# Performance work log

Measured on AMD Instinct MI355X. Metric: run time of the kernel, lower is better.

Reference implementation:

```python
import jax, jax.numpy as jnp
import numpy as np

N_NODES = 100000
N_EDGES = 600000
FEAT = 128
N_RELS = 8


def setup_inputs() -> dict:
    key = jax.random.key(0)
    k1, k2, k3, k4, k5, k6, k7 = jax.random.split(key, 7)
    return {
        "h": jax.random.normal(k1, (N_NODES, FEAT), dtype=jnp.float32),
        "weight": jax.random.normal(k2, (N_RELS, FEAT, FEAT), dtype=jnp.float32) * (1.0 / np.sqrt(FEAT)),
        "gate_weight": jax.random.normal(k3, (N_RELS, FEAT, 1), dtype=jnp.float32) * (1.0 / np.sqrt(FEAT)),
        "norm": jax.random.uniform(k4, (N_EDGES, 1), dtype=jnp.float32),
        "src": jax.random.randint(k5, (N_EDGES,), 0, N_NODES, dtype=jnp.int32),
        "dst": jax.random.randint(k6, (N_EDGES,), 0, N_NODES, dtype=jnp.int32),
        "rel_type": jax.random.randint(k7, (N_EDGES,), 0, N_RELS, dtype=jnp.int32),
    }


def reference(h, weight, gate_weight, norm, src, dst, rel_type):
    # Transform every node by every relation once: [N, R, F].
    # Mathematically identical to per-edge bmm h_src @ W[rel], but avoids
    # materializing an [E, F, F] gathered weight tensor.
    h_all = jnp.einsum('nd,rdf->nrf', h, weight)            # [N, R, F]
    gate_all = jnp.einsum('nd,rdo->nro', h, gate_weight)[..., 0]  # [N, R]

    msg = h_all[src, rel_type] * norm                        # [E, F]
    gate = jax.nn.sigmoid(gate_all[src, rel_type])[:, None]  # [E, 1]
    msg = msg * gate

    out = jax.ops.segment_sum(msg, dst, num_segments=h.shape[0])  # scatter-sum to dst nodes
    return jax.nn.relu(out)
```

## Files before the change

### kernel.cpp

```cpp
#include <hip/hip_runtime.h>
#include <hip/hip_bf16.h>

#define FEAT 128
#define NRELS 8
#define KTOT 1024
#define BN 32
#define ECAP 256
#define CPAD 16

typedef __bf16 bf16_t;
typedef __bf16 bf16x2_t __attribute__((ext_vector_type(2)));
typedef __bf16 bf16x8_t __attribute__((ext_vector_type(8)));
typedef float f32x4 __attribute__((ext_vector_type(4)));

struct __align__(8) PackedEdge { int row; float scale; };

static inline size_t align256(size_t x) { return (x + 255) & ~(size_t)255; }

__global__ __launch_bounds__(256) void k_prep(
    const float* __restrict__ h, const float* __restrict__ gwt,
    const float* __restrict__ w, float* __restrict__ sg,
    bf16_t* __restrict__ hb, bf16_t* __restrict__ wt2,
    int* __restrict__ cur, int N, int nbk) {
    const int t = threadIdx.x;
    const int gid = blockIdx.x * 256 + t;
    const int nthreads = gridDim.x * 256;
    for (int i = gid; i < NRELS * FEAT * FEAT; i += nthreads) {
        int r = i >> 14;
        int rem = i & 16383;
        int d = rem >> 7;
        int f = rem & 127;
        wt2[(size_t)f * KTOT + r * FEAT + d] = (bf16_t)w[i];
    }
    for (int i = gid; i < nbk * CPAD + 1; i += nthreads) cur[i] = 0;

    const int gw_id = gid >> 6;
    const int nwaves = nthreads >> 6;
    const int lane = t & 63;
    for (int node = gw_id; node < N; node += nwaves) {
        float2 hv2 = *reinterpret_cast<const float2*>(h + (size_t)node * FEAT + lane * 2);
        bf16x2_t hc;
        hc.x = (bf16_t)hv2.x;
        hc.y = (bf16_t)hv2.y;
        *reinterpret_cast<bf16x2_t*>(hb + (size_t)node * FEAT + lane * 2) = hc;

        int r = lane >> 3;
        int g = lane & 7;
        const float4* hp = reinterpret_cast<const float4*>(h + (size_t)node * FEAT + g * 16);
        const float4* wp = reinterpret_cast<const float4*>(gwt + r * FEAT + g * 16);
        float s = 0.f;
#pragma unroll
        for (int i = 0; i < 4; ++i) {
            float4 a = hp[i];
            float4 b = wp[i];
            s += a.x * b.x + a.y * b.y + a.z * b.z + a.w * b.w;
        }
        s += __shfl_xor(s, 1, 64);
        s += __shfl_xor(s, 2, 64);
        s += __shfl_xor(s, 4, 64);
        if (g == 0) sg[(size_t)node * NRELS + r] = 1.0f / (1.0f + __expf(-s));
    }
}

__global__ void k_fills(const int* __restrict__ src, const int* __restrict__ dstv,
                        const int* __restrict__ rel, const float* __restrict__ nrm,
                        const float* __restrict__ sg, int* __restrict__ cur,
                        PackedEdge* __restrict__ slab, PackedEdge* __restrict__ ovfrec,
                        int* __restrict__ ovfbk, int* __restrict__ ovfcnt, int nedges) {
    int e = blockIdx.x * blockDim.x + threadIdx.x;
    if (e >= nedges) return;
    int d = dstv[e];
    int s = src[e];
    int r = rel[e];
    int bk = d >> 5;
    PackedEdge p;
    p.row = (s << 8) | ((d & 31) << 3) | r;
    p.scale = nrm[e] * sg[(size_t)s * NRELS + r];
    int pos = atomicAdd(&cur[bk * CPAD], 1);
    if (pos < ECAP) {
        slab[(size_t)bk * ECAP + pos] = p;
    } else {
        int op = atomicAdd(ovfcnt, 1);
        ovfrec[op] = p;
        ovfbk[op] = bk;
    }
}

__global__ __launch_bounds__(512, 4) void k_aggemm(const bf16_t* __restrict__ hb,
                                                   const bf16_t* __restrict__ wt2,
                                                   const PackedEdge* __restrict__ slab,
                                                   const int* __restrict__ cur,
                                                   const PackedEdge* __restrict__ ovfrec,
                                                   const int* __restrict__ ovfbk,
                                                   const int* __restrict__ ovfcnt,
                                                   float* __restrict__ out, int nnodes) {
    __shared__ __align__(16) char lds_raw[BN * KTOT * sizeof(bf16_t)];
    __shared__ __align__(8) PackedEdge elist[ECAP];
    __shared__ int kcnt[256];
    __shared__ int kbase[257];
    __shared__ int kwork[256];
    float* cst = (float*)lds_raw;
    const int t = threadIdx.x;
    const int nb0 = blockIdx.x * BN;
    const int lane = t & 63;
    const int wv = t >> 6;
    const int l15 = lane & 15;
    const int lhi = lane >> 4;

    const bf16_t* bp = wt2 + (size_t)(wv * 16 + l15) * KTOT + lhi * 8;
    bf16x8_t bv0 = *reinterpret_cast<const bf16x8_t*>(bp);
    bf16x8_t bv1 = *reinterpret_cast<const bf16x8_t*>(bp + 32);
    bf16x8_t bv2 = *reinterpret_cast<const bf16x8_t*>(bp + 64);
    bf16x8_t bv3 = *reinterpret_cast<const bf16x8_t*>(bp + 96);

    {
        f32x4 z = {0.f, 0.f, 0.f, 0.f};
#pragma unroll
        for (int i = 0; i < 8; ++i)
            reinterpret_cast<f32x4*>(lds_raw)[t + i * 512] = z;
    }

    const int cnt = cur[blockIdx.x * CPAD];
    const int nE = cnt < ECAP ? cnt : ECAP;
    if (t < 256) kcnt[t] = 0;
    __syncthreads();

    PackedEdge myrec = {0, 0.f};
    if (t < nE) {
        myrec = slab[(size_t)blockIdx.x * ECAP + t];
        atomicAdd(&kcnt[myrec.row & 255], 1);
    }
    __syncthreads();

    if (t < 64) {
        int c0 = kcnt[t * 4], c1 = kcnt[t * 4 + 1];
        int c2 = kcnt[t * 4 + 2], c3 = kcnt[t * 4 + 3];
        int tot = c0 + c1 + c2 + c3;
        int incl = tot;
#pragma unroll
        for (int off = 1; off < 64; off <<= 1) {
            int y = __shfl_up(incl, off, 64);
            if (t >= off) incl += y;
        }
        int excl = incl - tot;
        kbase[t * 4] = excl;               kwork[t * 4] = excl;
        kbase[t * 4 + 1] = excl + c0;      kwork[t * 4 + 1] = excl + c0;
        kbase[t * 4 + 2] = excl + c0 + c1; kwork[t * 4 + 2] = excl + c0 + c1;
        kbase[t * 4 + 3] = excl + c0 + c1 + c2;
        kwork[t * 4 + 3] = excl + c0 + c1 + c2;
        if (t == 63) kbase[256] = excl + tot;
    }
    __syncthreads();

    if (t < nE) elist[atomicAdd(&kwork[myrec.row & 255], 1)] = myrec;
    __syncthreads();

    {
        const int g2 = t >> 3;
        const int node = g2 >> 1;
        const int cidx = ((g2 & 1) << 3) | (t & 7);
        const int sw = node & 15;
        const int jbeg = kbase[node * 8];
        const int jend = kbase[node * 8 + 8];
        if (jbeg < jend) {
            float a[8];
#pragma unroll
            for (int i = 0; i < 8; ++i) a[i] = 0.f;
            int cur_r;

            auto ldrec = [&](int idx) {
                return elist[idx < jend ? idx : jend - 1];
            };
            auto ldrow = [&](const PackedEdge& p) {
                return *reinterpret_cast<const bf16x8_t*>(
                    hb + ((size_t)(p.row >> 8) << 7) + cidx * 8);
            };
            auto flush = [&](int rr) {
                int chunk = (rr * 16 + cidx) ^ sw;
                bf16_t* dp = reinterpret_cast<bf16_t*>(
                    lds_raw + (size_t)node * 2048 + chunk * 16);
                bf16x8_t old = *reinterpret_cast<const bf16x8_t*>(dp);
                bf16x8_t o;
#pragma unroll
                for (int i = 0; i < 8; ++i) o[i] = (bf16_t)((float)old[i] + a[i]);
                *reinterpret_cast<bf16x8_t*>(dp) = o;
            };
            auto consume = [&](const PackedEdge& p, const bf16x8_t& v, int idx) {
                if (idx < jend) {
                    int r = p.row & 7;
                    if (r != cur_r) {
                        flush(cur_r);
#pragma unroll
                        for (int i = 0; i < 8; ++i) a[i] = 0.f;
                        cur_r = r;
                    }
                    float s = p.scale;
#pragma unroll
                    for (int i = 0; i < 8; ++i) a[i] += (float)v[i] * s;
                }
            };

            PackedEdge p0 = ldrec(jbeg), p1 = ldrec(jbeg + 1);
            PackedEdge p2 = ldrec(jbeg + 2), p3 = ldrec(jbeg + 3);
            PackedEdge q0 = ldrec(jbeg + 4), q1 = ldrec(jbeg + 5);
            PackedEdge q2 = ldrec(jbeg + 6), q3 = ldrec(jbeg + 7);
            bf16x8_t v0 = ldrow(p0);
            bf16x8_t v1 = ldrow(p1);
            bf16x8_t v2 = ldrow(p2);
            bf16x8_t v3 = ldrow(p3);
            cur_r = p0.row & 7;

#pragma unroll 1
            for (int j = jbeg; j < jend; j += 4) {
                PackedEdge r0 = ldrec(j + 8), r1 = ldrec(j + 9);
                PackedEdge r2 = ldrec(j + 10), r3 = ldrec(j + 11);
                consume(p0, v0, j);
                consume(p1, v1, j + 1);
                consume(p2, v2, j + 2);
                consume(p3, v3, j + 3);
                v0 = ldrow(q0); v1 = ldrow(q1); v2 = ldrow(q2); v3 = ldrow(q3);
                p0 = q0; p1 = q1; p2 = q2; p3 = q3;
                q0 = r0; q1 = r1; q2 = r2; q3 = r3;
            }
            flush(cur_r);
        }

        int novf = *ovfcnt;
        if (novf > 0) {
#pragma unroll 1
            for (int i = 0; i < novf; ++i) {
                if (ovfbk[i] != blockIdx.x) continue;
                PackedEdge p = ovfrec[i];
                if (((p.row >> 3) & 31) != node) continue;
                bf16x8_t v = *reinterpret_cast<const bf16x8_t*>(
                    hb + ((size_t)(p.row >> 8) << 7) + cidx * 8);
                int chunk = ((p.row & 7) * 16 + cidx) ^ sw;
                bf16_t* dp = reinterpret_cast<bf16_t*>(
                    lds_raw + (size_t)node * 2048 + chunk * 16);
                bf16x8_t old = *reinterpret_cast<const bf16x8_t*>(dp);
                bf16x8_t o;
#pragma unroll
                for (int k = 0; k < 8; ++k)
                    o[k] = (bf16_t)((float)old[k] + (float)v[k] * p.scale);
                *reinterpret_cast<bf16x8_t*>(dp) = o;
            }
        }
    }
    __syncthreads();

    f32x4 acc0 = {0.f, 0.f, 0.f, 0.f};
    f32x4 acc1 = {0.f, 0.f, 0.f, 0.f};
    const char* a0p = lds_raw + (size_t)l15 * 2048;
    const char* a1p = a0p + 16 * 2048;
    const int swb = l15;

#define PB_STEP(I, BV)                                                         \
    {                                                                          \
        int ks = ks0 + (I);                                                    \
        int coff = ((ks * 4 + lhi) ^ swb) << 4;                                \
        bf16x8_t av0 = *reinterpret_cast<const bf16x8_t*>(a0p + coff);         \
        bf16x8_t av1 = *reinterpret_cast<const bf16x8_t*>(a1p + coff);         \
        bf16x8_t nxt = *reinterpret_cast<const bf16x8_t*>(                     \
            bp + (((ks + 4) & 31) * 32));                                      \
        acc0 = __builtin_amdgcn_mfma_f32_16x16x32_bf16(av0, BV, acc0, 0, 0, 0);\
        acc1 = __builtin_amdgcn_mfma_f32_16x16x32_bf16(av1, BV, acc1, 0, 0, 0);\
        BV = nxt;                                                              \
    }

#pragma unroll 1
    for (int ks0 = 0; ks0 < 32; ks0 += 4) {
        PB_STEP(0, bv0)
        PB_STEP(1, bv1)
        PB_STEP(2, bv2)
        PB_STEP(3, bv3)
    }
#undef PB_STEP
    __syncthreads();

    {
        int f = wv * 16 + l15;
#pragma unroll
        for (int i = 0; i < 4; ++i) {
            int n0 = lhi * 4 + i;
            cst[n0 * 132 + f] = acc0[i];
            cst[(n0 + 16) * 132 + f] = acc1[i];
        }
    }
    __syncthreads();

    {
        int node = t >> 4;
        int f0 = (t & 15) * 8;
        int gnode = nb0 + node;
        if (gnode < nnodes) {
            const float* cr = cst + node * 132 + f0;
            float4 o0, o1;
            o0.x = fmaxf(cr[0], 0.f); o0.y = fmaxf(cr[1], 0.f);
            o0.z = fmaxf(cr[2], 0.f); o0.w = fmaxf(cr[3], 0.f);
            o1.x = fmaxf(cr[4], 0.f); o1.y = fmaxf(cr[5], 0.f);
            o1.z = fmaxf(cr[6], 0.f); o1.w = fmaxf(cr[7], 0.f);
            float4* op = reinterpret_cast<float4*>(out + (size_t)gnode * FEAT + f0);
            op[0] = o0;
            op[1] = o1;
        }
    }
}

extern "C" void kernel_launch(void* const* d_in, const int* in_sizes, int n_in,
                              void* d_out, int out_size, void* d_ws, size_t ws_size,
                              hipStream_t stream) {
    const float* h = (const float*)d_in[0];
    const float* w = (const float*)d_in[1];
    const float* gwt = (const float*)d_in[2];
    const float* nrm = (const float*)d_in[3];
    const int* src = (const int*)d_in[4];
    const int* dst = (const int*)d_in[5];
    const int* rel = (const int*)d_in[6];
    float* out = (float*)d_out;

    const int N = in_sizes[0] / FEAT;
    const int E = in_sizes[4];
    const int nbk = (N + BN - 1) / BN;

    char* ws = (char*)d_ws;
    const size_t wt2B = align256((size_t)FEAT * KTOT * sizeof(bf16_t));
    const size_t hbB  = align256((size_t)N * FEAT * sizeof(bf16_t));
    const size_t sgB  = align256((size_t)N * NRELS * sizeof(float));
    const size_t cuB  = align256(((size_t)nbk * CPAD + 1) * sizeof(int));
    const size_t slB  = align256((size_t)nbk * ECAP * sizeof(PackedEdge));
    const size_t ovB  = align256((size_t)E * sizeof(PackedEdge));

    bf16_t* wt2 = (bf16_t*)ws;
    bf16_t* hb = (bf16_t*)(ws + wt2B);
    float* sg = (float*)(ws + wt2B + hbB);
    int* cur = (int*)(ws + wt2B + hbB + sgB);
    int* ovfcnt = cur + (size_t)nbk * CPAD;
    PackedEdge* slab = (PackedEdge*)(ws + wt2B + hbB + sgB + cuB);
    PackedEdge* ovfrec = (PackedEdge*)(ws + wt2B + hbB + sgB + cuB + slB);
    int* ovfbk = (int*)(ws + wt2B + hbB + sgB + cuB + slB + ovB);

    k_prep<<<4096, 256, 0, stream>>>(h, gwt, w, sg, hb, wt2, cur, N, nbk);
    k_fills<<<(E + 255) / 256, 256, 0, stream>>>(src, dst, rel, nrm, sg, cur, slab,
                                                 ovfrec, ovfbk, ovfcnt, E);
    k_aggemm<<<nbk, 512, 0, stream>>>(hb, wt2, slab, cur, ovfrec, ovfbk, ovfcnt,
                                      out, N);
}
```

Baseline: 294.0 us.

## Halve destination-node tile to 16 and rework gather lanes and weight transpose

Shrinks the per-block destination tile from 32 to 16 nodes, with a smaller edge capacity and a 7-bit row packing. Each wave now does one MFMA accumulator instead of two, and the gather gives each node 32 lanes that each load 4 bf16 values. This halves LDS per block so more blocks fit per CU and the grid grows, at the cost of reloading the 1024x128 weight fragments for twice as many blocks. The weight-transpose prep loop now writes contiguously and reads strided.

```diff
diff --git a/kernel.cpp b/kernel.cpp
--- a/kernel.cpp
+++ b/kernel.cpp
@@ -4,12 +4,13 @@
 #define FEAT 128
 #define NRELS 8
 #define KTOT 1024
-#define BN 32
-#define ECAP 256
+#define BN 16
+#define ECAP 192
 #define CPAD 16
 
 typedef __bf16 bf16_t;
 typedef __bf16 bf16x2_t __attribute__((ext_vector_type(2)));
+typedef __bf16 bf16x4_t __attribute__((ext_vector_type(4)));
 typedef __bf16 bf16x8_t __attribute__((ext_vector_type(8)));
 typedef float f32x4 __attribute__((ext_vector_type(4)));
 
@@ -26,11 +27,11 @@
     const int gid = blockIdx.x * 256 + t;
     const int nthreads = gridDim.x * 256;
     for (int i = gid; i < NRELS * FEAT * FEAT; i += nthreads) {
-        int r = i >> 14;
-        int rem = i & 16383;
-        int d = rem >> 7;
-        int f = rem & 127;
-        wt2[(size_t)f * KTOT + r * FEAT + d] = (bf16_t)w[i];
+        int f = i >> 10;
+        int k = i & 1023;
+        int r = k >> 7;
+        int d = k & 127;
+        wt2[i] = (bf16_t)w[(r << 14) + (d << 7) + f];
     }
     for (int i = gid; i < nbk * CPAD + 1; i += nthreads) cur[i] = 0;
 
@@ -72,9 +73,9 @@
     int d = dstv[e];
     int s = src[e];
     int r = rel[e];
-    int bk = d >> 5;
+    int bk = d >> 4;
     PackedEdge p;
-    p.row = (s << 8) | ((d & 31) << 3) | r;
+    p.row = (s << 7) | ((d & 15) << 3) | r;
     p.scale = nrm[e] * sg[(size_t)s * NRELS + r];
     int pos = atomicAdd(&cur[bk * CPAD], 1);
     if (pos < ECAP) {
@@ -96,9 +97,9 @@
                                                    float* __restrict__ out, int nnodes) {
     __shared__ __align__(16) char lds_raw[BN * KTOT * sizeof(bf16_t)];
     __shared__ __align__(8) PackedEdge elist[ECAP];
-    __shared__ int kcnt[256];
-    __shared__ int kbase[257];
-    __shared__ int kwork[256];
+    __shared__ int kcnt[128];
+    __shared__ int kbase[129];
+    __shared__ int kwork[128];
     float* cst = (float*)lds_raw;
     const int t = threadIdx.x;
     const int nb0 = blockIdx.x * BN;
@@ -116,26 +117,25 @@
     {
         f32x4 z = {0.f, 0.f, 0.f, 0.f};
 #pragma unroll
-        for (int i = 0; i < 8; ++i)
+        for (int i = 0; i < 4; ++i)
             reinterpret_cast<f32x4*>(lds_raw)[t + i * 512] = z;
     }
 
     const int cnt = cur[blockIdx.x * CPAD];
     const int nE = cnt < ECAP ? cnt : ECAP;
-    if (t < 256) kcnt[t] = 0;
+    if (t < 128) kcnt[t] = 0;
     __syncthreads();
 
     PackedEdge myrec = {0, 0.f};
     if (t < nE) {
         myrec = slab[(size_t)blockIdx.x * ECAP + t];
-        atomicAdd(&kcnt[myrec.row & 255], 1);
+        atomicAdd(&kcnt[myrec.row & 127], 1);
     }
     __syncthreads();
 
     if (t < 64) {
-        int c0 = kcnt[t * 4], c1 = kcnt[t * 4 + 1];
-        int c2 = kcnt[t * 4 + 2], c3 = kcnt[t * 4 + 3];
-        int tot = c0 + c1 + c2 + c3;
+        int c0 = kcnt[t * 2], c1 = kcnt[t * 2 + 1];
+        int tot = c0 + c1;
         int incl = tot;
 #pragma unroll
         for (int off = 1; off < 64; off <<= 1) {
@@ -143,60 +143,56 @@
             if (t >= off) incl += y;
         }
         int excl = incl - tot;
-        kbase[t * 4] = excl;               kwork[t * 4] = excl;
-        kbase[t * 4 + 1] = excl + c0;      kwork[t * 4 + 1] = excl + c0;
-        kbase[t * 4 + 2] = excl + c0 + c1; kwork[t * 4 + 2] = excl + c0 + c1;
-        kbase[t * 4 + 3] = excl + c0 + c1 + c2;
-        kwork[t * 4 + 3] = excl + c0 + c1 + c2;
-        if (t == 63) kbase[256] = excl + tot;
-    }
-    __syncthreads();
-
-    if (t < nE) elist[atomicAdd(&kwork[myrec.row & 255], 1)] = myrec;
+        kbase[t * 2] = excl;          kwork[t * 2] = excl;
+        kbase[t * 2 + 1] = excl + c0; kwork[t * 2 + 1] = excl + c0;
+        if (t == 63) kbase[128] = excl + tot;
+    }
+    __syncthreads();
+
+    if (t < nE) elist[atomicAdd(&kwork[myrec.row & 127], 1)] = myrec;
     __syncthreads();
 
     {
-        const int g2 = t >> 3;
-        const int node = g2 >> 1;
-        const int cidx = ((g2 & 1) << 3) | (t & 7);
-        const int sw = node & 15;
+        const int node = t >> 5;
+        const int c8 = t & 31;
+        const int sw = node;
         const int jbeg = kbase[node * 8];
         const int jend = kbase[node * 8 + 8];
         if (jbeg < jend) {
-            float a[8];
-#pragma unroll
-            for (int i = 0; i < 8; ++i) a[i] = 0.f;
+            float a[4];
+#pragma unroll
+            for (int i = 0; i < 4; ++i) a[i] = 0.f;
             int cur_r;
 
             auto ldrec = [&](int idx) {
                 return elist[idx < jend ? idx : jend - 1];
             };
             auto ldrow = [&](const PackedEdge& p) {
-                return *reinterpret_cast<const bf16x8_t*>(
-                    hb + ((size_t)(p.row >> 8) << 7) + cidx * 8);
+                return *reinterpret_cast<const bf16x4_t*>(
+                    hb + ((size_t)(p.row >> 7) << 7) + c8 * 4);
             };
             auto flush = [&](int rr) {
-                int chunk = (rr * 16 + cidx) ^ sw;
+                int chunk = (rr * 16 + (c8 >> 1)) ^ sw;
                 bf16_t* dp = reinterpret_cast<bf16_t*>(
-                    lds_raw + (size_t)node * 2048 + chunk * 16);
-                bf16x8_t old = *reinterpret_cast<const bf16x8_t*>(dp);
-                bf16x8_t o;
-#pragma unroll
-                for (int i = 0; i < 8; ++i) o[i] = (bf16_t)((float)old[i] + a[i]);
-                *reinterpret_cast<bf16x8_t*>(dp) = o;
+                    lds_raw + (size_t)node * 2048 + chunk * 16 + (c8 & 1) * 8);
+                bf16x4_t old = *reinterpret_cast<const bf16x4_t*>(dp);
+                bf16x4_t o;
+#pragma unroll
+                for (int i = 0; i < 4; ++i) o[i] = (bf16_t)((float)old[i] + a[i]);
+                *reinterpret_cast<bf16x4_t*>(dp) = o;
             };
-            auto consume = [&](const PackedEdge& p, const bf16x8_t& v, int idx) {
+            auto consume = [&](const PackedEdge& p, const bf16x4_t& v, int idx) {
                 if (idx < jend) {
                     int r = p.row & 7;
                     if (r != cur_r) {
                         flush(cur_r);
 #pragma unroll
-                        for (int i = 0; i < 8; ++i) a[i] = 0.f;
+                        for (int i = 0; i < 4; ++i) a[i] = 0.f;
                         cur_r = r;
                     }
                     float s = p.scale;
 #pragma unroll
-                    for (int i = 0; i < 8; ++i) a[i] += (float)v[i] * s;
+                    for (int i = 0; i < 4; ++i) a[i] += (float)v[i] * s;
                 }
             };
 
@@ -204,10 +200,10 @@
             PackedEdge p2 = ldrec(jbeg + 2), p3 = ldrec(jbeg + 3);
             PackedEdge q0 = ldrec(jbeg + 4), q1 = ldrec(jbeg + 5);
             PackedEdge q2 = ldrec(jbeg + 6), q3 = ldrec(jbeg + 7);
-            bf16x8_t v0 = ldrow(p0);
-            bf16x8_t v1 = ldrow(p1);
-            bf16x8_t v2 = ldrow(p2);
-            bf16x8_t v3 = ldrow(p3);
+            bf16x4_t v0 = ldrow(p0);
+            bf16x4_t v1 = ldrow(p1);
+            bf16x4_t v2 = ldrow(p2);
+            bf16x4_t v3 = ldrow(p3);
             cur_r = p0.row & 7;
 
 #pragma unroll 1
@@ -231,27 +227,25 @@
             for (int i = 0; i < novf; ++i) {
                 if (ovfbk[i] != blockIdx.x) continue;
                 PackedEdge p = ovfrec[i];
-                if (((p.row >> 3) & 31) != node) continue;
-                bf16x8_t v = *reinterpret_cast<const bf16x8_t*>(
-                    hb + ((size_t)(p.row >> 8) << 7) + cidx * 8);
-                int chunk = ((p.row & 7) * 16 + cidx) ^ sw;
+                if (((p.row >> 3) & 15) != node) continue;
+                bf16x4_t v = *reinterpret_cast<const bf16x4_t*>(
+                    hb + ((size_t)(p.row >> 7) << 7) + c8 * 4);
+                int chunk = ((p.row & 7) * 16 + (c8 >> 1)) ^ sw;
                 bf16_t* dp = reinterpret_cast<bf16_t*>(
-                    lds_raw + (size_t)node * 2048 + chunk * 16);
-                bf16x8_t old = *reinterpret_cast<const bf16x8_t*>(dp);
-                bf16x8_t o;
-#pragma unroll
-                for (int k = 0; k < 8; ++k)
+                    lds_raw + (size_t)node * 2048 + chunk * 16 + (c8 & 1) * 8);
+                bf16x4_t old = *reinterpret_cast<const bf16x4_t*>(dp);
+                bf16x4_t o;
+#pragma unroll
+                for (int k = 0; k < 4; ++k)
                     o[k] = (bf16_t)((float)old[k] + (float)v[k] * p.scale);
-                *reinterpret_cast<bf16x8_t*>(dp) = o;
+                *reinterpret_cast<bf16x4_t*>(dp) = o;
             }
         }
     }
     __syncthreads();
 
     f32x4 acc0 = {0.f, 0.f, 0.f, 0.f};
-    f32x4 acc1 = {0.f, 0.f, 0.f, 0.f};
     const char* a0p = lds_raw + (size_t)l15 * 2048;
-    const char* a1p = a0p + 16 * 2048;
     const int swb = l15;
 
 #define PB_STEP(I, BV)                                                         \
@@ -259,11 +253,9 @@
         int ks = ks0 + (I);                                                    \
         int coff = ((ks * 4 + lhi) ^ swb) << 4;                                \
         bf16x8_t av0 = *reinterpret_cast<const bf16x8_t*>(a0p + coff);         \
-        bf16x8_t av1 = *reinterpret_cast<const bf16x8_t*>(a1p + coff);         \
         bf16x8_t nxt = *reinterpret_cast<const bf16x8_t*>(                     \
             bp + (((ks + 4) & 31) * 32));                                      \
         acc0 = __builtin_amdgcn_mfma_f32_16x16x32_bf16(av0, BV, acc0, 0, 0, 0);\
-        acc1 = __builtin_amdgcn_mfma_f32_16x16x32_bf16(av1, BV, acc1, 0, 0, 0);\
         BV = nxt;                                                              \
     }
 
@@ -283,25 +275,22 @@
         for (int i = 0; i < 4; ++i) {
             int n0 = lhi * 4 + i;
             cst[n0 * 132 + f] = acc0[i];
-            cst[(n0 + 16) * 132 + f] = acc1[i];
         }
     }
     __syncthreads();
 
     {
-        int node = t >> 4;
-        int f0 = (t & 15) * 8;
+        int node = t >> 5;
+        int f0 = (t & 31) * 4;
         int gnode = nb0 + node;
         if (gnode < nnodes) {
             const float* cr = cst + node * 132 + f0;
-            float4 o0, o1;
-            o0.x = fmaxf(cr[0], 0.f); o0.y = fmaxf(cr[1], 0.f);
-            o0.z = fmaxf(cr[2], 0.f); o0.w = fmaxf(cr[3], 0.f);
-            o1.x = fmaxf(cr[4], 0.f); o1.y = fmaxf(cr[5], 0.f);
-            o1.z = fmaxf(cr[6], 0.f); o1.w = fmaxf(cr[7], 0.f);
-            float4* op = reinterpret_cast<float4*>(out + (size_t)gnode * FEAT + f0);
-            op[0] = o0;
-            op[1] = o1;
+            float4 o;
+            o.x = fmaxf(cr[0], 0.f);
+            o.y = fmaxf(cr[1], 0.f);
+            o.z = fmaxf(cr[2], 0.f);
+            o.w = fmaxf(cr[3], 0.f);
+            *reinterpret_cast<float4*>(out + (size_t)gnode * FEAT + f0) = o;
         }
     }
 }
```

Measured after the change: 390.8 us. 1.33x slower.
